# Kernel optimization log

Hardware: AMD Instinct MI355X
Metric: run time of the kernel (lower is better)

The kernel has to match this reference:

```python
import jax, jax.numpy as jnp
import numpy as np

N, E, HID, H, L, EF = 50000, 640000, 128, 8, 3, 16
C = HID // H  # 16, per-head output channels (concat=True)
NEG_SLOPE = 0.2
LN_EPS = 1e-5


def setup_inputs() -> dict:
    key = jax.random.key(0)
    ks = jax.random.split(key, 12)
    s = 0.05
    x = jax.random.normal(ks[0], (N, HID), jnp.float32)
    batch_index = jnp.sort(jax.random.randint(ks[1], (N,), 0, 64, dtype=jnp.int32))
    edge_index = jax.random.randint(ks[2], (2, E), 0, N, dtype=jnp.int32)
    edge_attr = jax.random.normal(ks[3], (E, EF), jnp.float32)
    # edge_transform: Linear(EF, HID)
    Wt = jax.random.normal(ks[4], (EF, HID), jnp.float32) * s
    bt = jnp.zeros((HID,), jnp.float32)
    # per-layer GATv2 params (stacked over L layers)
    Wl = jax.random.normal(ks[5], (L, HID, HID), jnp.float32) * s  # lin_l (source)
    bl = jnp.zeros((L, HID), jnp.float32)
    Wr = jax.random.normal(ks[6], (L, HID, HID), jnp.float32) * s  # lin_r (target)
    br = jnp.zeros((L, HID), jnp.float32)
    We = jax.random.normal(ks[7], (L, HID, HID), jnp.float32) * s  # lin_edge (no bias)
    att = jax.random.normal(ks[8], (L, H, C), jnp.float32) * s
    bias_o = jnp.zeros((L, HID), jnp.float32)
    ln_g = jnp.ones((L, HID), jnp.float32)
    ln_b = jnp.zeros((L, HID), jnp.float32)
    return dict(x=x, batch_index=batch_index, edge_index=edge_index, edge_attr=edge_attr,
                Wt=Wt, bt=bt, Wl=Wl, bl=bl, Wr=Wr, br=br, We=We, att=att,
                bias_o=bias_o, ln_g=ln_g, ln_b=ln_b)


def _layer_norm(x, g, b):
    mu = jnp.mean(x, axis=-1, keepdims=True)
    var = jnp.var(x, axis=-1, keepdims=True)
    return g * (x - mu) * jax.lax.rsqrt(var + LN_EPS) + b


def _gatv2_layer(x, ea, src, dst, Wl, bl, Wr, br, We, att, bias_o):
    # node transforms: lin_l for source features, lin_r for target features
    xl = (x @ Wl + bl).reshape(N, H, C)
    xr = (x @ Wr + br).reshape(N, H, C)
    em = (ea @ We).reshape(E, H, C)
    # per-edge attention logits (GATv2: leaky_relu AFTER the sum, then dot with att)
    m = jax.nn.leaky_relu(xl[src] + xr[dst] + em, NEG_SLOPE)  # [E,H,C]
    logits = jnp.einsum('ehc,hc->eh', m, att)                  # [E,H]
    # segment softmax over incoming edges of each destination node
    lmax = jax.ops.segment_max(logits, dst, num_segments=N)    # [N,H]
    p = jnp.exp(logits - lmax[dst])
    denom = jax.ops.segment_sum(p, dst, num_segments=N)        # [N,H]
    alpha = p / (denom[dst] + 1e-16)
    # weighted scatter-aggregate of source messages
    out = jax.ops.segment_sum(xl[src] * alpha[:, :, None], dst, num_segments=N)  # [N,H,C]
    return out.reshape(N, HID) + bias_o


def reference(x, batch_index, edge_index, edge_attr, Wt, bt, Wl, bl, Wr, br, We, att, bias_o, ln_g, ln_b):
    src, dst = edge_index[0], edge_index[1]
    ea = edge_attr @ Wt + bt  # shared edge_transform, [E,HID]
    for l in range(L):
        out = _gatv2_layer(x, ea, src, dst, Wl[l], bl[l], Wr[l], br[l], We[l], att[l], bias_o[l])
        out = _layer_norm(out, ln_g[l], ln_b[l])
        x = jax.nn.relu(out) + x  # dropout p=0 -> identity; residual
    return x
```

## Files before the change

kernel.cpp:

```cpp
#include <hip/hip_runtime.h>

#define N_NODES 50000
#define N_EDGES 640000
#define HID 128
#define EF 16
#define NLAYERS 3
#define CHUNK 32
#define SCAN_BLOCKS 196

typedef __attribute__((ext_vector_type(8))) short short8;
typedef __attribute__((ext_vector_type(4))) float f32x4;
typedef __attribute__((ext_vector_type(2))) float f32x2;

__device__ __forceinline__ unsigned short f2bf(float f) {
  unsigned int u = __float_as_uint(f);
  u = u + 0x7FFFu + ((u >> 16) & 1u);
  return (unsigned short)(u >> 16);
}

__device__ __forceinline__ float dpp_hadd8(float v) {
  int x;
  x = __builtin_amdgcn_update_dpp(0, __float_as_int(v), 0xB1, 0xF, 0xF, true);
  v += __int_as_float(x);
  x = __builtin_amdgcn_update_dpp(0, __float_as_int(v), 0x4E, 0xF, 0xF, true);
  v += __int_as_float(x);
  x = __builtin_amdgcn_update_dpp(0, __float_as_int(v), 0x141, 0xF, 0xF, true);
  v += __int_as_float(x);
  return v;
}

__device__ __forceinline__ int pslot(int j) {
  return (((j >> 4) * 8 + (j & 7)) << 1) + ((j >> 3) & 1);
}

__global__ __launch_bounds__(256) void k_setup(const float* __restrict__ Wt,
                                               const float* __restrict__ bt,
                                               const float* __restrict__ We,
                                               const float* __restrict__ Wl,
                                               const float* __restrict__ Wr,
                                               const float* __restrict__ x,
                                               float* __restrict__ Mt,
                                               float* __restrict__ ct,
                                               unsigned short* __restrict__ WT,
                                               unsigned short* __restrict__ xbf) {
  int b = blockIdx.x, t = threadIdx.x;
  if (b < 26) {
    int id = b * 256 + t;
    const int total = NLAYERS * (EF + 1) * HID;
    if (id >= total) return;
    int l = id / ((EF + 1) * HID);
    int r = id % ((EF + 1) * HID);
    int row = r / HID;
    int j = r % HID;
    const float* Wel = We + l * HID * HID;
    float s = 0.f;
    if (row < EF) {
      const float* wtr = Wt + row * HID;
      for (int i = 0; i < HID; ++i) s += wtr[i] * Wel[i * HID + j];
      Mt[(l * EF + row) * HID + pslot(j)] = s;
    } else {
      for (int i = 0; i < HID; ++i) s += bt[i] * Wel[i * HID + j];
      ct[l * HID + pslot(j)] = s;
    }
  } else if (b < 410) {
    int id = (b - 26) * 256 + t;
    int k = id & (HID - 1);
    int n = (id >> 7) & (HID - 1);
    int s = (id >> 14) & 1;
    int l = id >> 15;
    const float* W = (s == 0 ? Wl : Wr) + (size_t)l * HID * HID;
    WT[id] = f2bf(W[k * HID + n]);
  } else {
    int id = (b - 410) * 256 + t;
    const float4* p = (const float4*)(x + (size_t)id * 8);
    float4 a = p[0], bb = p[1];
    unsigned short o[8] = {f2bf(a.x), f2bf(a.y), f2bf(a.z), f2bf(a.w),
                           f2bf(bb.x), f2bf(bb.y), f2bf(bb.z), f2bf(bb.w)};
    *(uint4*)(xbf + (size_t)id * 8) = *(uint4*)o;
  }
}

__global__ __launch_bounds__(256) void k_hist(const int* __restrict__ dst, int* __restrict__ counts) {
  int e = blockIdx.x * 256 + threadIdx.x;
  if (e < N_EDGES) atomicAdd(&counts[dst[e]], 1);
}

__global__ __launch_bounds__(256) void k_scan1(const int* __restrict__ counts,
                                               int* __restrict__ rowptr,
                                               int* __restrict__ bsum) {
  __shared__ int sc[256];
  int t = threadIdx.x;
  int i = blockIdx.x * 256 + t;
  int v = (i < N_NODES) ? counts[i] : 0;
  sc[t] = v;
  __syncthreads();
  for (int off = 1; off < 256; off <<= 1) {
    int u = 0;
    if (t >= off) u = sc[t - off];
    __syncthreads();
    sc[t] += u;
    __syncthreads();
  }
  if (i < N_NODES) rowptr[i] = sc[t] - v;
  if (t == 255) bsum[blockIdx.x] = sc[255];
}

__global__ __launch_bounds__(256) void k_scan2(int* __restrict__ bsum) {
  __shared__ int sc[256];
  int t = threadIdx.x;
  int v = (t < SCAN_BLOCKS) ? bsum[t] : 0;
  sc[t] = v;
  __syncthreads();
  for (int off = 1; off < 256; off <<= 1) {
    int u = 0;
    if (t >= off) u = sc[t - off];
    __syncthreads();
    sc[t] += u;
    __syncthreads();
  }
  bsum[t] = sc[t] - v;
}

__global__ __launch_bounds__(256) void k_scan3(int* __restrict__ rowptr, const int* __restrict__ bsum) {
  int t = threadIdx.x;
  int i = blockIdx.x * 256 + t;
  if (i < N_NODES) rowptr[i] += bsum[blockIdx.x];
  if (i == 0) rowptr[N_NODES] = N_EDGES;
}

__global__ __launch_bounds__(256) void k_fill(const int* __restrict__ src,
                                              const int* __restrict__ dst,
                                              const int* __restrict__ rowptr,
                                              int* __restrict__ fill,
                                              int* __restrict__ ssrc,
                                              const float* __restrict__ eattr,
                                              float* __restrict__ easrt) {
  int e = blockIdx.x * 256 + threadIdx.x;
  if (e >= N_EDGES) return;
  int d = dst[e];
  int pos = atomicAdd(&fill[d], 1);
  int idx = rowptr[d] + pos;
  ssrc[idx] = src[e] << 6;
  const float4* pe = (const float4*)(eattr + (size_t)e * EF);
  float4* po = (float4*)(easrt + (size_t)idx * EF);
#pragma unroll
  for (int q = 0; q < 4; ++q) po[q] = pe[q];
}

__global__ __launch_bounds__(256) void k_gemm_mfma(const unsigned short* __restrict__ xbf,
                                                   const unsigned short* __restrict__ WTl,
                                                   const float* __restrict__ bl,
                                                   const float* __restrict__ br,
                                                   const float* __restrict__ ctl,
                                                   unsigned short* __restrict__ xlb,
                                                   unsigned short* __restrict__ xrb) {
  __shared__ short As[64 * 136];
  __shared__ short Bs[128 * 136];
  int t = threadIdx.x;
  int s = blockIdx.y;
  int row0 = blockIdx.x * 64;

  const uint4* gx = (const uint4*)xbf;
#pragma unroll
  for (int p = 0; p < 4; ++p) {
    int c = t + p * 256;
    int row = c >> 4, col16 = c & 15;
    int grow = row0 + row;
    if (grow >= N_NODES) grow = N_NODES - 1;
    uint4 v = gx[grow * 16 + col16];
    *(uint4*)(&As[row * 136 + col16 * 8]) = v;
  }
  const uint4* gw = (const uint4*)WTl;
#pragma unroll
  for (int p = 0; p < 8; ++p) {
    int c = t + p * 256;
    int row = c >> 4, col16 = c & 15;
    uint4 v = gw[s * 2048 + row * 16 + col16];
    *(uint4*)(&Bs[row * 136 + col16 * 8]) = v;
  }
  __syncthreads();

  int lane = t & 63, w = t >> 6;
  int quad = lane >> 4, lm = lane & 15;
  f32x4 acc[4][2];
#pragma unroll
  for (int mf = 0; mf < 4; ++mf)
#pragma unroll
    for (int nf = 0; nf < 2; ++nf) acc[mf][nf] = (f32x4)(0.f);

#pragma unroll
  for (int ks = 0; ks < 4; ++ks) {
    short8 af[4], bf[2];
#pragma unroll
    for (int mf = 0; mf < 4; ++mf)
      af[mf] = *(short8*)(&As[(mf * 16 + lm) * 136 + ks * 32 + quad * 8]);
#pragma unroll
    for (int nf = 0; nf < 2; ++nf)
      bf[nf] = *(short8*)(&Bs[(w * 32 + nf * 16 + lm) * 136 + ks * 32 + quad * 8]);
#pragma unroll
    for (int mf = 0; mf < 4; ++mf)
#pragma unroll
      for (int nf = 0; nf < 2; ++nf)
        acc[mf][nf] = __builtin_amdgcn_mfma_f32_16x16x32_bf16(af[mf], bf[nf], acc[mf][nf], 0, 0, 0);
  }

  const float* bias = (s == 0) ? bl : br;
  unsigned short* out = (s == 0) ? xlb : xrb;
#pragma unroll
  for (int nf = 0; nf < 2; ++nf) {
    int n = w * 32 + nf * 16 + lm;
    int slot = pslot(n);
    float bv = bias[n] + ((s == 1) ? ctl[slot] : 0.f);
#pragma unroll
    for (int mf = 0; mf < 4; ++mf) {
#pragma unroll
      for (int r = 0; r < 4; ++r) {
        int grow = row0 + mf * 16 + quad * 4 + r;
        if (grow < N_NODES) out[(size_t)grow * HID + slot] = f2bf(acc[mf][nf][r] + bv);
      }
    }
  }
}

__global__ __launch_bounds__(64) void k_fused(const float* __restrict__ xin,
                                              const unsigned int* __restrict__ xlb,
                                              const unsigned int* __restrict__ xrb,
                                              const int* __restrict__ rowptr,
                                              const int* __restrict__ ssrc,
                                              const float* __restrict__ easrt,
                                              const float* __restrict__ Mt,
                                              const float* __restrict__ att,
                                              const float* __restrict__ bias_o,
                                              const float* __restrict__ lng,
                                              const float* __restrict__ lnb,
                                              float* __restrict__ xout,
                                              unsigned short* __restrict__ xbf_out) {
  __shared__ __align__(16) float ea_s[CHUNK][EF];
  __shared__ int src_s[CHUNK + 8];
  int n = blockIdx.x;
  int l = threadIdx.x;
  int j0 = (l >> 3) * 16 + (l & 7), j1 = j0 + 8;

  f32x2 mtp[EF];
#pragma unroll
  for (int k = 0; k < EF; ++k) mtp[k] = *(const f32x2*)(&Mt[k * HID + l * 2]);
  unsigned int ur = xrb[(size_t)n * 64 + l];
  f32x2 base;
  base.x = __uint_as_float(ur << 16);
  base.y = __uint_as_float(ur & 0xFFFF0000u);
  const float LOG2E = 1.44269504088896340736f;
  f32x2 attp = {att[j0] * LOG2E, att[j1] * LOG2E};
  int beg = rowptr[n], end = rowptr[n + 1];

  f32x2 acc = {0.f, 0.f};
  float denom = 0.f;

  for (int c0 = beg; c0 < end; c0 += CHUNK) {
    int cnt = min(CHUNK, end - c0);
    if (l < cnt) src_s[l] = ssrc[c0 + l];
    if (l < 8) src_s[cnt + l] = 0;
    for (int q = l; q < cnt * 4; q += 64) {
      int i = q >> 2, part = q & 3;
      *(float4*)(&ea_s[i][part * 4]) =
          *(const float4*)(easrt + (size_t)(c0 + i) * EF + part * 4);
    }

    auto edge = [&](int i, unsigned int u) {
      f32x2 xls;
      xls.x = __uint_as_float(u << 16);
      xls.y = __uint_as_float(u & 0xFFFF0000u);
      f32x2 m = base + xls;
      const f32x4* er = (const f32x4*)(&ea_s[i][0]);
      f32x4 e0 = er[0], e1 = er[1], e2 = er[2], e3 = er[3];
#pragma unroll
      for (int k = 0; k < 4; ++k) m += e0[k] * mtp[k];
#pragma unroll
      for (int k = 0; k < 4; ++k) m += e1[k] * mtp[4 + k];
#pragma unroll
      for (int k = 0; k < 4; ++k) m += e2[k] * mtp[8 + k];
#pragma unroll
      for (int k = 0; k < 4; ++k) m += e3[k] * mtp[12 + k];
      f32x2 am = {__int_as_float(__float_as_int(m.x) & 0x7FFFFFFF),
                  __int_as_float(__float_as_int(m.y) & 0x7FFFFFFF)};
      m = 0.6f * m + 0.4f * am;
      f32x2 v2 = m * attp;
      float vs = dpp_hadd8(v2.x + v2.y);
      float p = exp2f(vs);
      denom += p;
      acc += xls * p;
    };

    unsigned int cur[4];
#pragma unroll
    for (int q = 0; q < 4; ++q) cur[q] = xlb[src_s[q] + l];
    int cnt4 = cnt & ~3;
    for (int i = 0; i < cnt4; i += 4) {
      unsigned int nxt[4];
#pragma unroll
      for (int q = 0; q < 4; ++q) nxt[q] = xlb[src_s[i + 4 + q] + l];
#pragma unroll
      for (int q = 0; q < 4; ++q) edge(i + q, cur[q]);
#pragma unroll
      for (int q = 0; q < 4; ++q) cur[q] = nxt[q];
    }
#pragma unroll
    for (int q = 0; q < 4; ++q)
      if (cnt4 + q < cnt) edge(cnt4 + q, cur[q]);
  }

  f32x2 outp;
  float inv = 1.f / (denom + 1e-16f);
  outp.x = acc.x * inv + bias_o[j0];
  outp.y = acc.y * inv + bias_o[j1];
  float s1 = outp.x + outp.y;
  float s2 = outp.x * outp.x + outp.y * outp.y;
#pragma unroll
  for (int mask = 1; mask <= 32; mask <<= 1) {
    s1 += __shfl_xor(s1, mask);
    s2 += __shfl_xor(s2, mask);
  }
  float mu = s1 * (1.f / 128.f);
  float var = s2 * (1.f / 128.f) - mu * mu;
  float rs = rsqrtf(var + 1e-5f);
  float y0 = lng[j0] * (outp.x - mu) * rs + lnb[j0];
  float y1 = lng[j1] * (outp.y - mu) * rs + lnb[j1];
  float r0 = fmaxf(y0, 0.f) + xin[(size_t)n * HID + j0];
  float r1 = fmaxf(y1, 0.f) + xin[(size_t)n * HID + j1];
  xout[(size_t)n * HID + j0] = r0;
  xout[(size_t)n * HID + j1] = r1;
  xbf_out[(size_t)n * HID + j0] = f2bf(r0);
  xbf_out[(size_t)n * HID + j1] = f2bf(r1);
}

extern "C" void kernel_launch(void* const* d_in, const int* in_sizes, int n_in,
                              void* d_out, int out_size, void* d_ws, size_t ws_size,
                              hipStream_t stream) {
  const float* x0    = (const float*)d_in[0];
  const int*   eidx  = (const int*)d_in[2];
  const float* eattr = (const float*)d_in[3];
  const float* Wt    = (const float*)d_in[4];
  const float* bt    = (const float*)d_in[5];
  const float* Wl    = (const float*)d_in[6];
  const float* bl    = (const float*)d_in[7];
  const float* Wr    = (const float*)d_in[8];
  const float* br    = (const float*)d_in[9];
  const float* We    = (const float*)d_in[10];
  const float* att   = (const float*)d_in[11];
  const float* bo    = (const float*)d_in[12];
  const float* lng   = (const float*)d_in[13];
  const float* lnb   = (const float*)d_in[14];
  float* out = (float*)d_out;
  const int* src = eidx;
  const int* dst = eidx + N_EDGES;

  char* ws = (char*)d_ws;
  size_t off = 0;
  auto alloc = [&](size_t bytes) {
    char* p = ws + off;
    off += (bytes + 255) & ~(size_t)255;
    return p;
  };
  int* counts = (int*)alloc((size_t)N_NODES * 4);
  int* fill   = (int*)((char*)counts + (size_t)N_NODES * 4);
  fill = (int*)alloc((size_t)N_NODES * 4);
  float* Mt   = (float*)alloc((size_t)NLAYERS * EF * HID * 4);
  float* ct   = (float*)alloc((size_t)NLAYERS * HID * 4);
  int* rowptr = (int*)alloc((size_t)(N_NODES + 1) * 4);
  int* bsum   = (int*)alloc(256 * 4);
  int* ssrc   = (int*)alloc((size_t)N_EDGES * 4);
  float* easrt = (float*)alloc((size_t)N_EDGES * EF * 4);
  unsigned short* xlb = (unsigned short*)alloc((size_t)N_NODES * HID * 2);
  unsigned short* xrb = (unsigned short*)alloc((size_t)N_NODES * HID * 2);
  float* xbuf = (float*)alloc((size_t)N_NODES * HID * 4);
  unsigned short* xbf = (unsigned short*)alloc((size_t)N_NODES * HID * 2);
  unsigned short* WTb = (unsigned short*)alloc((size_t)NLAYERS * 2 * HID * HID * 2);

  hipMemsetAsync(counts, 0, (char*)(fill + N_NODES) - (char*)counts, stream);

  hipLaunchKernelGGL(k_setup, dim3(3535), dim3(256), 0, stream,
                     Wt, bt, We, Wl, Wr, x0, Mt, ct, WTb, xbf);
  hipLaunchKernelGGL(k_hist, dim3((N_EDGES + 255) / 256), dim3(256), 0, stream, dst, counts);
  hipLaunchKernelGGL(k_scan1, dim3(SCAN_BLOCKS), dim3(256), 0, stream, counts, rowptr, bsum);
  hipLaunchKernelGGL(k_scan2, dim3(1), dim3(256), 0, stream, bsum);
  hipLaunchKernelGGL(k_scan3, dim3(SCAN_BLOCKS), dim3(256), 0, stream, rowptr, bsum);
  hipLaunchKernelGGL(k_fill, dim3((N_EDGES + 255) / 256), dim3(256), 0, stream,
                     src, dst, rowptr, fill, ssrc, eattr, easrt);

  for (int l = 0; l < NLAYERS; ++l) {
    const float* xin = (l == 0) ? x0 : (const float*)xbuf;
    float* xout = (l == NLAYERS - 1) ? out : xbuf;
    hipLaunchKernelGGL(k_gemm_mfma, dim3((N_NODES + 63) / 64, 2), dim3(256), 0, stream,
                       xbf, WTb + (size_t)l * 2 * HID * HID, bl + l * HID, br + l * HID,
                       ct + (size_t)l * HID, xlb, xrb);
    hipLaunchKernelGGL(k_fused, dim3(N_NODES), dim3(64), 0, stream,
                       xin, (const unsigned int*)xlb, (const unsigned int*)xrb,
                       rowptr, ssrc, easrt,
                       Mt + (size_t)l * EF * HID, att + l * HID,
                       bo + l * HID, lng + l * HID, lnb + l * HID, xout, xbf);
  }
}
```

Measured before the change: 471.7 us.

## Compute per-edge edge-feature projection with fp16 MFMA per chunk

Measured after the change: 441.3 us. 6.4% less time.

```diff
diff --git a/kernel.cpp b/kernel.cpp
--- a/kernel.cpp
+++ b/kernel.cpp
@@ -5,10 +5,11 @@
 #define HID 128
 #define EF 16
 #define NLAYERS 3
-#define CHUNK 32
+#define CHUNK 16
 #define SCAN_BLOCKS 196
 
 typedef __attribute__((ext_vector_type(8))) short short8;
+typedef __attribute__((ext_vector_type(8))) _Float16 half8;
 typedef __attribute__((ext_vector_type(4))) float f32x4;
 typedef __attribute__((ext_vector_type(2))) float f32x2;
 
@@ -16,6 +17,11 @@
   unsigned int u = __float_as_uint(f);
   u = u + 0x7FFFu + ((u >> 16) & 1u);
   return (unsigned short)(u >> 16);
+}
+
+__device__ __forceinline__ unsigned short f2h(float f) {
+  _Float16 h = (_Float16)f;
+  return *(unsigned short*)&h;
 }
 
 __device__ __forceinline__ float dpp_hadd8(float v) {
@@ -29,6 +35,17 @@
   return v;
 }
 
+__device__ __forceinline__ f32x2 pk_add(f32x2 a, f32x2 b) {
+  f32x2 d;
+  asm("v_pk_add_f32 %0, %1, %2" : "=v"(d) : "v"(a), "v"(b));
+  return d;
+}
+__device__ __forceinline__ f32x2 pk_mul(f32x2 a, f32x2 b) {
+  f32x2 d;
+  asm("v_pk_mul_f32 %0, %1, %2" : "=v"(d) : "v"(a), "v"(b));
+  return d;
+}
+
 __device__ __forceinline__ int pslot(int j) {
   return (((j >> 4) * 8 + (j & 7)) << 1) + ((j >> 3) & 1);
 }
@@ -39,8 +56,8 @@
                                                const float* __restrict__ Wl,
                                                const float* __restrict__ Wr,
                                                const float* __restrict__ x,
-                                               float* __restrict__ Mt,
                                                float* __restrict__ ct,
+                                               unsigned short* __restrict__ MtB,
                                                unsigned short* __restrict__ WT,
                                                unsigned short* __restrict__ xbf) {
   int b = blockIdx.x, t = threadIdx.x;
@@ -57,7 +74,10 @@
     if (row < EF) {
       const float* wtr = Wt + row * HID;
       for (int i = 0; i < HID; ++i) s += wtr[i] * Wel[i * HID + j];
-      Mt[(l * EF + row) * HID + pslot(j)] = s;
+      int blk = j >> 4, nn = j & 15;
+      size_t base = (size_t)(l * 8 + blk) * 64;
+      MtB[(base + (size_t)((row >> 3) * 16 + nn)) * 8 + (row & 7)] = f2h(s);
+      MtB[(base + (size_t)((2 + (row >> 3)) * 16 + nn)) * 8 + (row & 7)] = 0;
     } else {
       for (int i = 0; i < HID; ++i) s += bt[i] * Wel[i * HID + j];
       ct[l * HID + pslot(j)] = s;
@@ -134,17 +154,25 @@
                                               int* __restrict__ fill,
                                               int* __restrict__ ssrc,
                                               const float* __restrict__ eattr,
-                                              float* __restrict__ easrt) {
+                                              unsigned short* __restrict__ eaA) {
   int e = blockIdx.x * 256 + threadIdx.x;
   if (e >= N_EDGES) return;
   int d = dst[e];
   int pos = atomicAdd(&fill[d], 1);
   int idx = rowptr[d] + pos;
   ssrc[idx] = src[e] << 6;
-  const float4* pe = (const float4*)(eattr + (size_t)e * EF);
-  float4* po = (float4*)(easrt + (size_t)idx * EF);
-#pragma unroll
-  for (int q = 0; q < 4; ++q) po[q] = pe[q];
+  const float* pe = eattr + (size_t)e * EF;
+  unsigned short* po = eaA + (size_t)idx * 32;
+#pragma unroll
+  for (int g = 0; g < 2; ++g) {
+    unsigned short o[8];
+#pragma unroll
+    for (int k = 0; k < 8; ++k) o[k] = f2h(pe[g * 8 + k]);
+    *(uint4*)(po + g * 8) = *(uint4*)o;
+  }
+  uint4 z = {0u, 0u, 0u, 0u};
+  *(uint4*)(po + 16) = z;
+  *(uint4*)(po + 24) = z;
 }
 
 __global__ __launch_bounds__(256) void k_gemm_mfma(const unsigned short* __restrict__ xbf,
@@ -227,29 +255,33 @@
                                               const unsigned int* __restrict__ xrb,
                                               const int* __restrict__ rowptr,
                                               const int* __restrict__ ssrc,
-                                              const float* __restrict__ easrt,
-                                              const float* __restrict__ Mt,
+                                              const unsigned short* __restrict__ eaA,
+                                              const unsigned int* __restrict__ MtBl,
                                               const float* __restrict__ att,
                                               const float* __restrict__ bias_o,
                                               const float* __restrict__ lng,
                                               const float* __restrict__ lnb,
                                               float* __restrict__ xout,
                                               unsigned short* __restrict__ xbf_out) {
-  __shared__ __align__(16) float ea_s[CHUNK][EF];
+  __shared__ __align__(16) float em_s[CHUNK * 130];
   __shared__ int src_s[CHUNK + 8];
   int n = blockIdx.x;
   int l = threadIdx.x;
+  int lm = l & 15, quad = l >> 4;
   int j0 = (l >> 3) * 16 + (l & 7), j1 = j0 + 8;
 
-  f32x2 mtp[EF];
-#pragma unroll
-  for (int k = 0; k < EF; ++k) mtp[k] = *(const f32x2*)(&Mt[k * HID + l * 2]);
+  uint4 bfr[8];
+  const uint4* mb = (const uint4*)MtBl;
+#pragma unroll
+  for (int b = 0; b < 8; ++b) bfr[b] = mb[b * 64 + l];
+
   unsigned int ur = xrb[(size_t)n * 64 + l];
   f32x2 base;
   base.x = __uint_as_float(ur << 16);
   base.y = __uint_as_float(ur & 0xFFFF0000u);
   const float LOG2E = 1.44269504088896340736f;
   f32x2 attp = {att[j0] * LOG2E, att[j1] * LOG2E};
+  f32x2 c02 = {0.2f, 0.2f};
   int beg = rowptr[n], end = rowptr[n + 1];
 
   f32x2 acc = {0.f, 0.f};
@@ -259,35 +291,33 @@
     int cnt = min(CHUNK, end - c0);
     if (l < cnt) src_s[l] = ssrc[c0 + l];
     if (l < 8) src_s[cnt + l] = 0;
-    for (int q = l; q < cnt * 4; q += 64) {
-      int i = q >> 2, part = q & 3;
-      *(float4*)(&ea_s[i][part * 4]) =
-          *(const float4*)(easrt + (size_t)(c0 + i) * EF + part * 4);
-    }
+
+    half8 af = *(const half8*)(eaA + (size_t)(c0 + lm) * 32 + quad * 8);
+    f32x4 cc[8];
+#pragma unroll
+    for (int b = 0; b < 8; ++b)
+      cc[b] = __builtin_amdgcn_mfma_f32_16x16x32_f16(af, *(half8*)&bfr[b], (f32x4)(0.f), 0, 0, 0);
+#pragma unroll
+    for (int b = 0; b < 8; ++b)
+#pragma unroll
+      for (int r = 0; r < 4; ++r)
+        em_s[(quad * 4 + r) * 130 + ((b * 8 + (lm & 7)) << 1) + (lm >> 3)] = cc[b][r];
 
     auto edge = [&](int i, unsigned int u) {
       f32x2 xls;
       xls.x = __uint_as_float(u << 16);
       xls.y = __uint_as_float(u & 0xFFFF0000u);
-      f32x2 m = base + xls;
-      const f32x4* er = (const f32x4*)(&ea_s[i][0]);
-      f32x4 e0 = er[0], e1 = er[1], e2 = er[2], e3 = er[3];
-#pragma unroll
-      for (int k = 0; k < 4; ++k) m += e0[k] * mtp[k];
-#pragma unroll
-      for (int k = 0; k < 4; ++k) m += e1[k] * mtp[4 + k];
-#pragma unroll
-      for (int k = 0; k < 4; ++k) m += e2[k] * mtp[8 + k];
-#pragma unroll
-      for (int k = 0; k < 4; ++k) m += e3[k] * mtp[12 + k];
-      f32x2 am = {__int_as_float(__float_as_int(m.x) & 0x7FFFFFFF),
-                  __int_as_float(__float_as_int(m.y) & 0x7FFFFFFF)};
-      m = 0.6f * m + 0.4f * am;
-      f32x2 v2 = m * attp;
+      f32x2 em = *(const f32x2*)(&em_s[i * 130 + 2 * l]);
+      f32x2 m = pk_add(pk_add(base, xls), em);
+      f32x2 ms = pk_mul(c02, m);
+      m.x = fmaxf(m.x, ms.x);
+      m.y = fmaxf(m.y, ms.y);
+      f32x2 v2 = pk_mul(m, attp);
       float vs = dpp_hadd8(v2.x + v2.y);
       float p = exp2f(vs);
       denom += p;
-      acc += xls * p;
+      acc.x = fmaf(xls.x, p, acc.x);
+      acc.y = fmaf(xls.y, p, acc.y);
     };
 
     unsigned int cur[4];
@@ -361,14 +391,13 @@
     return p;
   };
   int* counts = (int*)alloc((size_t)N_NODES * 4);
-  int* fill   = (int*)((char*)counts + (size_t)N_NODES * 4);
-  fill = (int*)alloc((size_t)N_NODES * 4);
-  float* Mt   = (float*)alloc((size_t)NLAYERS * EF * HID * 4);
+  int* fill   = (int*)alloc((size_t)N_NODES * 4);
   float* ct   = (float*)alloc((size_t)NLAYERS * HID * 4);
   int* rowptr = (int*)alloc((size_t)(N_NODES + 1) * 4);
   int* bsum   = (int*)alloc(256 * 4);
   int* ssrc   = (int*)alloc((size_t)N_EDGES * 4);
-  float* easrt = (float*)alloc((size_t)N_EDGES * EF * 4);
+  unsigned short* eaA = (unsigned short*)alloc(((size_t)N_EDGES + 16) * 32 * 2);
+  unsigned short* MtB = (unsigned short*)alloc((size_t)NLAYERS * 8 * 64 * 8 * 2);
   unsigned short* xlb = (unsigned short*)alloc((size_t)N_NODES * HID * 2);
   unsigned short* xrb = (unsigned short*)alloc((size_t)N_NODES * HID * 2);
   float* xbuf = (float*)alloc((size_t)N_NODES * HID * 4);
@@ -378,13 +407,13 @@
   hipMemsetAsync(counts, 0, (char*)(fill + N_NODES) - (char*)counts, stream);
 
   hipLaunchKernelGGL(k_setup, dim3(3535), dim3(256), 0, stream,
-                     Wt, bt, We, Wl, Wr, x0, Mt, ct, WTb, xbf);
+                     Wt, bt, We, Wl, Wr, x0, ct, MtB, WTb, xbf);
   hipLaunchKernelGGL(k_hist, dim3((N_EDGES + 255) / 256), dim3(256), 0, stream, dst, counts);
   hipLaunchKernelGGL(k_scan1, dim3(SCAN_BLOCKS), dim3(256), 0, stream, counts, rowptr, bsum);
   hipLaunchKernelGGL(k_scan2, dim3(1), dim3(256), 0, stream, bsum);
   hipLaunchKernelGGL(k_scan3, dim3(SCAN_BLOCKS), dim3(256), 0, stream, rowptr, bsum);
   hipLaunchKernelGGL(k_fill, dim3((N_EDGES + 255) / 256), dim3(256), 0, stream,
-                     src, dst, rowptr, fill, ssrc, eattr, easrt);
+                     src, dst, rowptr, fill, ssrc, eattr, eaA);
 
   for (int l = 0; l < NLAYERS; ++l) {
     const float* xin = (l == 0) ? x0 : (const float*)xbuf;
@@ -394,8 +423,9 @@
                        ct + (size_t)l * HID, xlb, xrb);
     hipLaunchKernelGGL(k_fused, dim3(N_NODES), dim3(64), 0, stream,
                        xin, (const unsigned int*)xlb, (const unsigned int*)xrb,
-                       rowptr, ssrc, easrt,
-                       Mt + (size_t)l * EF * HID, att + l * HID,
+                       rowptr, ssrc, eaA,
+                       (const unsigned int*)(MtB + (size_t)l * 8 * 64 * 8),
+                       att + l * HID,
                        bo + l * HID, lng + l * HID, lnb + l * HID, xout, xbf);
   }
 }
```
